# Kernel tuning notes

Measured on AMD Instinct MI355X. Metric: run time of the kernel, lower is better.

The kernel has to match this reference:

```python
import jax, jax.numpy as jnp
import numpy as np

B, L, D = 2, 2048, 1024
NUM_HEADS = 16
HEAD_DIM = D // NUM_HEADS


def setup_inputs() -> dict:
    key = jax.random.key(0)
    k1, k2 = jax.random.split(key)
    x = jax.random.normal(k1, (B, L, D), dtype=jnp.float32)
    # torch Linear(input_dim, 3*output_dim, bias=False); store as [in, 3*out] for x @ W
    W_qkv = jax.random.normal(k2, (D, 3 * D), dtype=jnp.float32) * (1.0 / np.sqrt(D))
    return {"x": x, "W_qkv": W_qkv}


def reference(x, W_qkv):
    b, l, d = x.shape
    h, hd = NUM_HEADS, HEAD_DIM
    qkv = x @ W_qkv                                  # [B, L, 3*D]
    qkv = qkv.reshape(b, l, 3, h, hd)
    q = jnp.transpose(qkv[:, :, 0], (0, 2, 1, 3))    # [B, H, L, hd]
    k = jnp.transpose(qkv[:, :, 1], (0, 2, 1, 3))
    v = jnp.transpose(qkv[:, :, 2], (0, 2, 1, 3))
    scale = 1.0 / jnp.sqrt(jnp.asarray(hd, dtype=x.dtype))
    scores = jnp.einsum('bhqd,bhkd->bhqk', q, k) * scale   # [B, H, L, L]
    causal = jnp.triu(jnp.ones((l, l), dtype=bool), k=1)   # True above diagonal -> masked
    scores = jnp.where(causal, -jnp.inf, scores)
    attn = jax.nn.softmax(scores, axis=-1)
    # dropout p=0.0 -> identity (eval mode)
    out = jnp.einsum('bhqk,bhkd->bhqd', attn, v)            # [B, H, L, hd]
    out = jnp.transpose(out, (0, 2, 1, 3)).reshape(b, l, h * hd)
    return out
```

## Files before the change

kernel.cpp:

```cpp
#include <hip/hip_runtime.h>
#include <hip/hip_bf16.h>
#include <math.h>

#define NB_L 2048
#define GM 4096
#define GN 3072
#define GK 1024
#define NROWS 65536
#define SCALE_L2E 0.180336880f

typedef float  f4v __attribute__((ext_vector_type(4)));
typedef short  s4v __attribute__((ext_vector_type(4)));
typedef short  s8v __attribute__((ext_vector_type(8)));

#define MFMA_16x16x32(a, b, c) __builtin_amdgcn_mfma_f32_16x16x32_bf16((a), (b), (c), 0, 0, 0)
#define MFMA_16x16x16(a, b, c) __builtin_amdgcn_mfma_f32_16x16x16bf16_1k((a), (b), (c), 0, 0, 0)

static __device__ __forceinline__ unsigned int bfpk(float a, float b) {
    __hip_bfloat162 h = __float22bfloat162_rn(float2{a, b});
    union { __hip_bfloat162 h2; unsigned int u; } cv; cv.h2 = h; return cv.u;
}
static __device__ __forceinline__ unsigned short bf1(float a) {
    union { __hip_bfloat16 h; unsigned short u; } cv; cv.h = __float2bfloat16(a); return cv.u;
}
static __device__ __forceinline__ float bf2f(unsigned short u) {
    union { unsigned int u; float f; } cv; cv.u = ((unsigned int)u) << 16; return cv.f;
}

static __device__ __forceinline__ void gl_lds16(const ushort* g, ushort* l) {
    __builtin_amdgcn_global_load_lds((const __attribute__((address_space(1))) void*)g,
                                     (__attribute__((address_space(3))) void*)l, 16, 0, 0);
}

__global__ __launch_bounds__(256) void conv_fused(
    const float* __restrict__ X, const float* __restrict__ W,
    ushort* __restrict__ Xb, ushort* __restrict__ Wt)
{
    __shared__ __align__(16) ushort T[64][72];
    const int bid = blockIdx.x, t = threadIdx.x;
    if (bid < 2048) {
        const int i = bid * 256 + t;
        const float4 f0 = ((const float4*)X)[2 * i];
        const float4 f1 = ((const float4*)X)[2 * i + 1];
        uint4 u;
        u.x = bfpk(f0.x, f0.y); u.y = bfpk(f0.z, f0.w);
        u.z = bfpk(f1.x, f1.y); u.w = bfpk(f1.z, f1.w);
        ((uint4*)Xb)[i] = u;
    } else {
        const int wb = bid - 2048;
        const int k0 = (wb & 15) * 64, n0 = (wb >> 4) * 64;
        {
            const int kr = t >> 2, nc0 = (t & 3) * 16;
            const float* src = W + (size_t)(k0 + kr) * GN + n0 + nc0;
#pragma unroll
            for (int u = 0; u < 4; ++u) {
                const float4 v = *(const float4*)(src + 4 * u);
                T[nc0 + 4 * u + 0][kr] = bf1(v.x);
                T[nc0 + 4 * u + 1][kr] = bf1(v.y);
                T[nc0 + 4 * u + 2][kr] = bf1(v.z);
                T[nc0 + 4 * u + 3][kr] = bf1(v.w);
            }
        }
        __syncthreads();
        {
            const int nr = t >> 2, kc0 = (t & 3) * 16;
            ushort* dst = Wt + (size_t)(n0 + nr) * GK + k0 + kc0;
            *(s8v*)dst       = *(const s8v*)&T[nr][kc0];
            *(s8v*)(dst + 8) = *(const s8v*)&T[nr][kc0 + 8];
        }
    }
}

__global__ __launch_bounds__(256, 4) void qkv_gemm_bf16(
    const ushort* __restrict__ Xb, const ushort* __restrict__ Wt,
    ushort* __restrict__ Qh, ushort* __restrict__ Kh, ushort* __restrict__ VT)
{
    __shared__ __align__(16) ushort As[2][4 * 128 * 8];
    __shared__ __align__(16) ushort Bs[2][4 * 128 * 8];
    const int tid = threadIdx.x;
    const int row0 = blockIdx.y * 128, col0 = blockIdx.x * 96;
    const int lane = tid & 63, w = tid >> 6;
    const int wr = w >> 1, wc = w & 1, lq = lane & 15, quad = lane >> 4;

    f4v acc[4][3];
#pragma unroll
    for (int g = 0; g < 4; ++g)
#pragma unroll
        for (int j = 0; j < 3; ++j) acc[g][j] = 0.f;

    const int sr = tid & 127;
    const bool bok = sr < 96;
    const ushort* gA1 = Xb + (size_t)(row0 + sr) * GK + (tid >> 7) * 8;
    const ushort* gA2 = gA1 + 16;
    const ushort* gB1 = Wt + (size_t)(col0 + sr) * GK + (tid >> 7) * 8;
    const ushort* gB2 = gB1 + 16;
    const int d1 = tid * 8, d2 = (tid + 256) * 8;

    gl_lds16(gA1, &As[0][d1]);
    gl_lds16(gA2, &As[0][d2]);
    if (bok) {
        gl_lds16(gB1, &Bs[0][d1]);
        gl_lds16(gB2, &Bs[0][d2]);
    }

    for (int it = 0; it < 32; ++it) {
        const int cur = it & 1, nxt = cur ^ 1;
        __syncthreads();
        if (it + 1 < 32) {
            const int k0 = (it + 1) * 32;
            gl_lds16(gA1 + k0, &As[nxt][d1]);
            gl_lds16(gA2 + k0, &As[nxt][d2]);
            if (bok) {
                gl_lds16(gB1 + k0, &Bs[nxt][d1]);
                gl_lds16(gB2 + k0, &Bs[nxt][d2]);
            }
        }
        s8v af[4], bfr[3];
#pragma unroll
        for (int g = 0; g < 4; ++g)
            af[g]  = *(const s8v*)&As[cur][(quad * 128 + wr * 64 + g * 16 + lq) * 8];
#pragma unroll
        for (int j = 0; j < 3; ++j)
            bfr[j] = *(const s8v*)&Bs[cur][(quad * 128 + wc * 48 + j * 16 + lq) * 8];
#pragma unroll
        for (int g = 0; g < 4; ++g)
#pragma unroll
            for (int j = 0; j < 3; ++j)
                acc[g][j] = MFMA_16x16x32(af[g], bfr[j], acc[g][j]);
    }

#pragma unroll
    for (int g = 0; g < 4; ++g)
#pragma unroll
        for (int j = 0; j < 3; ++j) {
            const int col = col0 + wc * 48 + j * 16 + lq;
            const int part = col >> 10, colp = col & 1023;
            const int hh = colp >> 6, d = colp & 63;
#pragma unroll
            for (int r = 0; r < 4; ++r) {
                const int row = row0 + wr * 64 + g * 16 + quad * 4 + r;
                const int b = row >> 11, tok = row & 2047;
                const int bh = b * 16 + hh;
                if (part == 0) {
                    Qh[((size_t)bh * 2048 + tok) * 64 + d] = bf1(acc[g][j][r] * SCALE_L2E);
                } else if (part == 1) {
                    Kh[((size_t)bh * 2048 + tok) * 64 + (d ^ ((tok & 7) << 3))] = bf1(acc[g][j][r]);
                } else {
                    VT[((size_t)bh * 64 + d) * 2048 + (tok ^ ((d & 7) << 3))] = bf1(acc[g][j][r]);
                }
            }
        }
}

__global__ __launch_bounds__(256, 4) void attn_bf16(
    const ushort* __restrict__ Qh, const ushort* __restrict__ Kh,
    const ushort* __restrict__ VT, ushort* __restrict__ Opart, float* __restrict__ Lp)
{
    __shared__ __align__(16) ushort Ks[2][64 * 64];
    __shared__ __align__(16) ushort Vt[2][64 * 64];

    const int x = blockIdx.x;
    const int bh = x & 31;
    const int qlow = (x >> 5) & 7;
    const int s = (x >> 8) & 1;
    const int x9 = (x >> 9) & 1;
    const int qt = x9 ? (15 - qlow) : qlow;

    const int tid = threadIdx.x;
    const int w = tid >> 6, lane = tid & 63;
    const int lq = lane & 15, quad = lane >> 4;
    const int kswz = (lq & 7) << 3;
    const int qrow_base = qt * 128 + w * 32;
    const int diag = 2 * qt + (w >> 1);

    s8v qf[2][2];
#pragma unroll
    for (int qg = 0; qg < 2; ++qg)
#pragma unroll
        for (int sb = 0; sb < 2; ++sb)
            qf[qg][sb] = *(const s8v*)(Qh + ((size_t)bh * 2048 + qrow_base + qg * 16 + lq) * 64
                                       + sb * 32 + quad * 8);

    f4v o[4][2];
#pragma unroll
    for (int dg = 0; dg < 4; ++dg)
#pragma unroll
        for (int qg = 0; qg < 2; ++qg) o[dg][qg] = 0.f;
    f4v lacc[2]; lacc[0] = 0.f; lacc[1] = 0.f;
    const s4v ones = { (short)0x3F80, (short)0x3F80, (short)0x3F80, (short)0x3F80 };

    const int kt_lo = s ? (qt + 1) : 0;
    const int kt_hi = s ? (2 * qt + 1) : qt;
    const int niter = kt_hi - kt_lo + 1;

    const ushort* kbase = Kh + (size_t)bh * 2048 * 64;
    const ushort* vbase = VT + (size_t)bh * 64 * 2048;
    const int g1 = tid, g2 = tid + 256;
    const int kr1 = g1 >> 3, ko1 = (g1 & 7) * 8;
    const int kr2 = g2 >> 3, ko2 = (g2 & 7) * 8;

    auto stage = [&](int kt, int bufi) {
        const ushort* kt_k = kbase + (size_t)kt * 64 * 64;
        const ushort* kt_v = vbase + kt * 64;
        gl_lds16(kt_k + kr1 * 64 + ko1,           &Ks[bufi][g1 * 8]);
        gl_lds16(kt_k + kr2 * 64 + ko2,           &Ks[bufi][g2 * 8]);
        gl_lds16(kt_v + (size_t)kr1 * 2048 + ko1, &Vt[bufi][g1 * 8]);
        gl_lds16(kt_v + (size_t)kr2 * 2048 + ko2, &Vt[bufi][g2 * 8]);
    };

    auto compute = [&](int ktc, int bufi) {
        if (ktc > diag) return;
        f4v st[4][2];
#pragma unroll
        for (int kg = 0; kg < 4; ++kg)
#pragma unroll
            for (int qg = 0; qg < 2; ++qg) st[kg][qg] = 0.f;
#pragma unroll
        for (int kg = 0; kg < 4; ++kg)
#pragma unroll
            for (int sb = 0; sb < 2; ++sb) {
                const s8v af = *(const s8v*)&Ks[bufi][(kg * 16 + lq) * 64
                                                     + ((sb * 32 + quad * 8) ^ kswz)];
#pragma unroll
                for (int qg = 0; qg < 2; ++qg)
                    st[kg][qg] = MFMA_16x16x32(af, qf[qg][sb], st[kg][qg]);
            }
        if (ktc == diag) {
#pragma unroll
            for (int kg = 0; kg < 4; ++kg)
#pragma unroll
                for (int qg = 0; qg < 2; ++qg) {
                    const int qrow = qrow_base + qg * 16 + lq;
#pragma unroll
                    for (int r = 0; r < 4; ++r)
                        if (ktc * 64 + kg * 16 + quad * 4 + r > qrow)
                            st[kg][qg][r] = -INFINITY;
                }
        }
#pragma unroll
        for (int kg = 0; kg < 4; ++kg)
#pragma unroll
            for (int qg = 0; qg < 2; ++qg)
#pragma unroll
                for (int r = 0; r < 4; ++r)
                    st[kg][qg][r] = exp2f(st[kg][qg][r]);
#pragma unroll
        for (int ks = 0; ks < 4; ++ks) {
            s4v pb[2];
#pragma unroll
            for (int qg = 0; qg < 2; ++qg) {
                union { s4v v; uint2 u; } c;
                c.u.x = bfpk(st[ks][qg][0], st[ks][qg][1]);
                c.u.y = bfpk(st[ks][qg][2], st[ks][qg][3]);
                pb[qg] = c.v;
            }
#pragma unroll
            for (int qg = 0; qg < 2; ++qg)
                lacc[qg] = MFMA_16x16x16(ones, pb[qg], lacc[qg]);
#pragma unroll
            for (int dg = 0; dg < 4; ++dg) {
                const s4v va = *(const s4v*)&Vt[bufi][(dg * 16 + lq) * 64
                                                     + ((ks * 16 + quad * 4) ^ kswz)];
#pragma unroll
                for (int qg = 0; qg < 2; ++qg)
                    o[dg][qg] = MFMA_16x16x16(va, pb[qg], o[dg][qg]);
            }
        }
    };

    stage(kt_lo, 0);
    for (int i = 0; i < niter; ++i) {
        const int cur = i & 1;
        __syncthreads();
        if (i + 1 < niter) stage(kt_lo + i + 1, cur ^ 1);
        compute(kt_lo + i, cur);
    }

#pragma unroll
    for (int qg = 0; qg < 2; ++qg) {
        const size_t prow = (size_t)(s * 32 + bh) * 2048 + qrow_base + qg * 16 + lq;
#pragma unroll
        for (int dg = 0; dg < 4; ++dg) {
            const int d = dg * 16 + quad * 4;
            uint2 u;
            u.x = bfpk(o[dg][qg][0], o[dg][qg][1]);
            u.y = bfpk(o[dg][qg][2], o[dg][qg][3]);
            *(uint2*)&Opart[prow * 64 + d] = u;
        }
        if (quad == 0) Lp[prow] = lacc[qg][0];
    }
}

__global__ __launch_bounds__(256) void attn_combine(
    const ushort* __restrict__ Opart, const float* __restrict__ Lp, float* __restrict__ Out)
{
    const int id = blockIdx.x * 256 + threadIdx.x;
    const int row = id >> 4, c4 = (id & 15) * 4;
    const float l0 = Lp[row], l1 = Lp[row + NROWS];
    const float inv = 1.0f / (l0 + l1);

    const s4v a = *(const s4v*)&Opart[(size_t)row * 64 + c4];
    const s4v c = *(const s4v*)&Opart[(size_t)(row + NROWS) * 64 + c4];
    float4 v;
    v.x = (bf2f((unsigned short)a[0]) + bf2f((unsigned short)c[0])) * inv;
    v.y = (bf2f((unsigned short)a[1]) + bf2f((unsigned short)c[1])) * inv;
    v.z = (bf2f((unsigned short)a[2]) + bf2f((unsigned short)c[2])) * inv;
    v.w = (bf2f((unsigned short)a[3]) + bf2f((unsigned short)c[3])) * inv;

    const int bh = row >> 11, qrow = row & 2047;
    const int b = bh >> 4, h = bh & 15;
    *(float4*)(Out + ((size_t)(b * 2048 + qrow)) * 1024 + h * 64 + c4) = v;
}

extern "C" void kernel_launch(void* const* d_in, const int* in_sizes, int n_in,
                              void* d_out, int out_size, void* d_ws, size_t ws_size,
                              hipStream_t stream)
{
    const float* x  = (const float*)d_in[0];
    const float* wq = (const float*)d_in[1];
    float* out = (float*)d_out;

    const size_t HEADTEN = (size_t)32 * 2048 * 64;
    ushort* wsp = (ushort*)d_ws;
    ushort* qh = wsp;
    ushort* kh = qh + HEADTEN;
    ushort* vt = kh + HEADTEN;
    ushort* xb = vt + HEADTEN;
    ushort* wt = xb + (size_t)GM * GK;
    ushort* opart = xb;
    float*  lp    = (float*)(opart + (size_t)2 * NROWS * 64);

    conv_fused<<<2816, 256, 0, stream>>>(x, wq, xb, wt);
    qkv_gemm_bf16<<<dim3(32, 32), 256, 0, stream>>>(xb, wt, qh, kh, vt);
    attn_bf16<<<1024, 256, 0, stream>>>(qh, kh, vt, opart, lp);
    attn_combine<<<NROWS * 16 / 256, 256, 0, stream>>>(opart, lp, out);
}
```

Baseline: 202.6 us.

## Load QKV GEMM fragments directly from global into registers, drop LDS staging

The QKV projection GEMM no longer stages tiles through shared memory with barriers. Each wave now loads its MFMA operand fragments straight from global memory into registers, double-buffered across k-steps. The block tile also grows from 128x96 to 128x128 (a 4x4 MFMA grid per wave), which shrinks the grid and lets the Q/K/V part be computed per block. This removes the LDS traffic and syncs, but each wave now re-reads A/B from global/L2 with no sharing inside the block, and the larger accumulator set raises register pressure.

```diff
diff --git a/kernel.cpp b/kernel.cpp
--- a/kernel.cpp
+++ b/kernel.cpp
@@ -71,70 +71,69 @@
     }
 }
 
-__global__ __launch_bounds__(256, 4) void qkv_gemm_bf16(
+__global__ __launch_bounds__(256) void qkv_gemm_bf16(
     const ushort* __restrict__ Xb, const ushort* __restrict__ Wt,
     ushort* __restrict__ Qh, ushort* __restrict__ Kh, ushort* __restrict__ VT)
 {
-    __shared__ __align__(16) ushort As[2][4 * 128 * 8];
-    __shared__ __align__(16) ushort Bs[2][4 * 128 * 8];
     const int tid = threadIdx.x;
-    const int row0 = blockIdx.y * 128, col0 = blockIdx.x * 96;
     const int lane = tid & 63, w = tid >> 6;
     const int wr = w >> 1, wc = w & 1, lq = lane & 15, quad = lane >> 4;
-
-    f4v acc[4][3];
+    const int row0 = blockIdx.y * 128, col0 = blockIdx.x * 128;
+
+    const ushort* pa[4];
+    const ushort* pb[4];
 #pragma unroll
     for (int g = 0; g < 4; ++g)
-#pragma unroll
-        for (int j = 0; j < 3; ++j) acc[g][j] = 0.f;
-
-    const int sr = tid & 127;
-    const bool bok = sr < 96;
-    const ushort* gA1 = Xb + (size_t)(row0 + sr) * GK + (tid >> 7) * 8;
-    const ushort* gA2 = gA1 + 16;
-    const ushort* gB1 = Wt + (size_t)(col0 + sr) * GK + (tid >> 7) * 8;
-    const ushort* gB2 = gB1 + 16;
-    const int d1 = tid * 8, d2 = (tid + 256) * 8;
-
-    gl_lds16(gA1, &As[0][d1]);
-    gl_lds16(gA2, &As[0][d2]);
-    if (bok) {
-        gl_lds16(gB1, &Bs[0][d1]);
-        gl_lds16(gB2, &Bs[0][d2]);
+        pa[g] = Xb + (size_t)(row0 + wr * 64 + g * 16 + lq) * GK + quad * 8;
+#pragma unroll
+    for (int j = 0; j < 4; ++j)
+        pb[j] = Wt + (size_t)(col0 + wc * 64 + j * 16 + lq) * GK + quad * 8;
+
+    f4v acc[4][4];
+#pragma unroll
+    for (int g = 0; g < 4; ++g)
+#pragma unroll
+        for (int j = 0; j < 4; ++j) acc[g][j] = 0.f;
+
+    s8v a0[4], b0[4], a1[4], b1[4];
+#pragma unroll
+    for (int g = 0; g < 4; ++g) { a0[g] = *(const s8v*)pa[g]; b0[g] = *(const s8v*)pb[g]; }
+
+    for (int it = 0; it < 32; it += 2) {
+        {
+            const int k0 = (it + 1) * 32;
+#pragma unroll
+            for (int g = 0; g < 4; ++g) {
+                a1[g] = *(const s8v*)(pa[g] + k0);
+                b1[g] = *(const s8v*)(pb[g] + k0);
+            }
+        }
+#pragma unroll
+        for (int g = 0; g < 4; ++g)
+#pragma unroll
+            for (int j = 0; j < 4; ++j)
+                acc[g][j] = MFMA_16x16x32(a0[g], b0[j], acc[g][j]);
+        if (it + 2 < 32) {
+            const int k0 = (it + 2) * 32;
+#pragma unroll
+            for (int g = 0; g < 4; ++g) {
+                a0[g] = *(const s8v*)(pa[g] + k0);
+                b0[g] = *(const s8v*)(pb[g] + k0);
+            }
+        }
+#pragma unroll
+        for (int g = 0; g < 4; ++g)
+#pragma unroll
+            for (int j = 0; j < 4; ++j)
+                acc[g][j] = MFMA_16x16x32(a1[g], b1[j], acc[g][j]);
     }
 
-    for (int it = 0; it < 32; ++it) {
-        const int cur = it & 1, nxt = cur ^ 1;
-        __syncthreads();
-        if (it + 1 < 32) {
-            const int k0 = (it + 1) * 32;
-            gl_lds16(gA1 + k0, &As[nxt][d1]);
-            gl_lds16(gA2 + k0, &As[nxt][d2]);
-            if (bok) {
-                gl_lds16(gB1 + k0, &Bs[nxt][d1]);
-                gl_lds16(gB2 + k0, &Bs[nxt][d2]);
-            }
-        }
-        s8v af[4], bfr[3];
-#pragma unroll
-        for (int g = 0; g < 4; ++g)
-            af[g]  = *(const s8v*)&As[cur][(quad * 128 + wr * 64 + g * 16 + lq) * 8];
-#pragma unroll
-        for (int j = 0; j < 3; ++j)
-            bfr[j] = *(const s8v*)&Bs[cur][(quad * 128 + wc * 48 + j * 16 + lq) * 8];
-#pragma unroll
-        for (int g = 0; g < 4; ++g)
-#pragma unroll
-            for (int j = 0; j < 3; ++j)
-                acc[g][j] = MFMA_16x16x32(af[g], bfr[j], acc[g][j]);
-    }
-
+    const int part = blockIdx.x >> 3;
 #pragma unroll
     for (int g = 0; g < 4; ++g)
 #pragma unroll
-        for (int j = 0; j < 3; ++j) {
-            const int col = col0 + wc * 48 + j * 16 + lq;
-            const int part = col >> 10, colp = col & 1023;
+        for (int j = 0; j < 4; ++j) {
+            const int colp = (col0 & 1023) + wc * 64 + j * 16 + lq;
             const int hh = colp >> 6, d = colp & 63;
 #pragma unroll
             for (int r = 0; r < 4; ++r) {
@@ -331,7 +330,7 @@
     float*  lp    = (float*)(opart + (size_t)2 * NROWS * 64);
 
     conv_fused<<<2816, 256, 0, stream>>>(x, wq, xb, wt);
-    qkv_gemm_bf16<<<dim3(32, 32), 256, 0, stream>>>(xb, wt, qh, kh, vt);
+    qkv_gemm_bf16<<<dim3(24, 32), 256, 0, stream>>>(xb, wt, qh, kh, vt);
     attn_bf16<<<1024, 256, 0, stream>>>(qh, kh, vt, opart, lp);
     attn_combine<<<NROWS * 16 / 256, 256, 0, stream>>>(opart, lp, out);
 }
```

Result: slower. 253.6 us (+25.2%).
